# Kernel optimization log

Measured on AMD Instinct MI355X. Metric: run time of the kernel, lower is better.

## Reference

```python
import jax, jax.numpy as jnp
import numpy as np

B, N, R, DIM = 4, 1024, 5, 1024
H, DH = 16, 64
ALPHA = 128.0
# FLAGS.fix_attention=True, a_sim=False: q * (dim_head**-0.5 * alpha**-1) * mult**-0.5
SCALE = (DH ** -0.5) * (1.0 / ALPHA) * (R ** -0.5)
EPS = 1e-5


def layernorm(x, g):
    mean = jnp.mean(x, axis=-1, keepdims=True)
    var = jnp.mean((x - mean) ** 2, axis=-1, keepdims=True)  # unbiased=False
    return (x - mean) * jax.lax.rsqrt(var + EPS) * g


def setup_inputs() -> dict:
    key = jax.random.key(0)
    ks = jax.random.split(key, 8)
    x = jax.random.normal(ks[0], (B, N, R, DIM), dtype=jnp.float32)
    mask = jax.random.bernoulli(ks[1], 0.9, (B, N))
    g_in = jnp.ones((DIM,), dtype=jnp.float32)
    Wq = jax.random.normal(ks[2], (DIM, H * DH), dtype=jnp.float32) * 0.02
    Wkv = jax.random.normal(ks[3], (DIM, 2 * DH), dtype=jnp.float32) * 0.02
    null_kv = jax.random.normal(ks[4], (2, DH), dtype=jnp.float32)
    Wout = jax.random.normal(ks[5], (H * DH, DIM), dtype=jnp.float32) * 0.02
    g_out = jnp.ones((DIM,), dtype=jnp.float32)
    return {"x": x, "mask": mask, "g_in": g_in, "Wq": Wq, "Wkv": Wkv,
            "null_kv": null_kv, "Wout": Wout, "g_out": g_out}


def reference(x, mask, g_in, Wq, Wkv, null_kv, Wout, g_out):
    # context defaults to the UN-normalized x (set before norm in the original)
    context = x
    xn = layernorm(x, g_in)                               # [b,n,r,dim]
    q = jnp.einsum('bnrc,ce->bnre', xn, Wq)               # [b,n,r,h*d]
    q = q.reshape(B, N, R, H, DH).transpose(0, 3, 1, 2, 4)  # b h n r d
    q = q * SCALE
    kv = jnp.einsum('bnrc,ce->bnre', context, Wkv)        # [b,n,r,2d] (multi-query: 1 kv head)
    k, v = kv[..., :DH], kv[..., DH:]                     # [b,n,r,d]
    # null kv token prepended along the j (sequence) axis, repeated over r
    nk = jnp.broadcast_to(null_kv[0], (B, 1, R, DH))
    nv = jnp.broadcast_to(null_kv[1], (B, 1, R, DH))
    k = jnp.concatenate([nk, k], axis=1)                  # [b,n+1,r,d]
    v = jnp.concatenate([nv, v], axis=1)
    sim = jnp.einsum('bhird,bjrd->bhij', q, k)            # [b,h,n,n+1]
    big = jnp.finfo(sim.dtype).max
    maskp = jnp.pad(mask, ((0, 0), (1, 0)), constant_values=True)  # null token always visible
    sim = jnp.where(maskp[:, None, None, :], sim, -big)
    # pb-relax: subtract detached row max, rescale by alpha
    sim = sim - jax.lax.stop_gradient(jnp.max(sim, axis=-1, keepdims=True))
    attn = jax.nn.softmax(sim * ALPHA, axis=-1)
    out = jnp.einsum('bhij,bjrd->bhird', attn, v)         # b h n r d
    out = out.transpose(0, 2, 3, 1, 4).reshape(B, N, R, H * DH)
    out = jnp.einsum('bnre,eo->bnro', out, Wout)
    return layernorm(out, g_out)
```

## Files before the change

### kernel.cpp

```cpp
#include <hip/hip_runtime.h>

#define B_   4
#define N_   1024
#define R_   5
#define DIM_ 1024
#define H_   16
#define DH_  64
#define NJ   1056
#define CDIM 320
#define MROWS (B_*N_*R_)

typedef unsigned int u32;
typedef unsigned short u16;
typedef __attribute__((ext_vector_type(8))) short bf16x8;
typedef __attribute__((ext_vector_type(4))) float f32x4;
typedef __attribute__((ext_vector_type(16))) float f32x16;

constexpr float SCALEA_ = 0.05590169943749474f;

__device__ __forceinline__ u16 f2bf(float f) {
  u32 u = __builtin_bit_cast(u32, f);
  u32 r = (u + 0x7fffu + ((u >> 16) & 1u)) >> 16;
  return (u16)r;
}
__device__ __forceinline__ u32 pack2(float lo, float hi) {
  return (u32)f2bf(lo) | ((u32)f2bf(hi) << 16);
}
__device__ __forceinline__ void gld_lds16(void* lds, const void* g) {
  __builtin_amdgcn_global_load_lds((const __attribute__((address_space(1))) u32*)g,
                                   (__attribute__((address_space(3))) u32*)lds, 16, 0, 0);
}

__global__ void mask_detect(const u32* __restrict__ m, int* __restrict__ flag) {
  int t = threadIdx.x;
  int fl = 0;
  for (int i = t; i < 1024; i += 256) {
    u32 wv = m[i];
    if (wv == 0x3f800000u) fl |= 4;
    else if (wv > 1u) fl |= 2;
    if ((i & 1) && wv == 1u) fl |= 1;
  }
  if (fl) atomicOr(flag, fl);
}

__global__ void build_bias(const void* __restrict__ mask, const int* __restrict__ flag,
                           float* __restrict__ biasg) {
  int idx = blockIdx.x * 256 + threadIdx.x;
  if (idx >= B_ * NJ) return;
  int b = idx / NJ, j = idx % NJ;
  int mv;
  if (j == 0) mv = 1;
  else if (j > N_) mv = 0;
  else {
    int fb = flag[0];
    int mode = (fb & 4) ? 2 : ((fb & 2) ? 1 : ((fb & 1) ? 0 : 3));
    int mi = b * N_ + (j - 1);
    if (mode == 0)      mv = ((const int*)mask)[mi] != 0;
    else if (mode == 1) mv = ((const unsigned char*)mask)[mi] != 0;
    else if (mode == 2) mv = ((const float*)mask)[mi] != 0.0f;
    else                mv = ((const int*)mask)[mi * 2] != 0;
  }
  biasg[idx] = mv ? 0.0f : -__builtin_inff();
}

__global__ void kvfill(const float* __restrict__ nullkv, u16* __restrict__ kg, u16* __restrict__ vTg) {
  int idx = blockIdx.x * 256 + threadIdx.x;
  if (idx >= B_ * 32 * CDIM) return;
  int c  = idx % CDIM;
  int jj = (idx / CDIM) & 31;
  int b  = idx / (CDIM * 32);
  int j  = (jj == 0) ? 0 : (1024 + jj);
  u16 kvv, vvv;
  if (jj == 0) { kvv = f2bf(nullkv[c & 63]); vvv = f2bf(nullkv[64 + (c & 63)]); }
  else         { kvv = 0; vvv = 0; }
  kg [(size_t)(b * NJ + j) * CDIM + c] = kvv;
  vTg[(((size_t)b * 33 + (j >> 5)) * CDIM + c) * 32 + (j & 31)] = vvv;
}

__global__ __launch_bounds__(256) void transpose_cast(const float* __restrict__ W,
                                                      u16* __restrict__ WT, int K, int Nn) {
  __shared__ float tile[32][33];
  int tx = threadIdx.x & 31, ty = threadIdx.x >> 5;
  int n0 = blockIdx.x * 32, k0 = blockIdx.y * 32;
  #pragma unroll
  for (int e = 0; e < 4; ++e)
    tile[ty + e * 8][tx] = W[(size_t)(k0 + ty + e * 8) * Nn + n0 + tx];
  __syncthreads();
  #pragma unroll
  for (int e = 0; e < 4; ++e)
    WT[(size_t)(n0 + ty + e * 8) * K + k0 + tx] = f2bf(tile[tx][ty + e * 8]);
}

__global__ __launch_bounds__(256) void ln_in(const float* __restrict__ x, const float* __restrict__ gin,
                                             u16* __restrict__ xn, u16* __restrict__ xb) {
  const size_t row = blockIdx.x;
  const int t = threadIdx.x, w = t >> 6, lane = t & 63;
  const float* xr = x + row * 1024;
  f32x4 v = *(const f32x4*)(xr + t * 4);
  float s = v[0] + v[1] + v[2] + v[3];
  #pragma unroll
  for (int o = 1; o < 64; o <<= 1) s += __shfl_xor(s, o);
  __shared__ float red[8];
  if (lane == 0) red[w] = s;
  __syncthreads();
  float mean = (red[0] + red[1] + red[2] + red[3]) * (1.0f / 1024.0f);
  f32x4 d;
  float ss = 0.f;
  #pragma unroll
  for (int e = 0; e < 4; ++e) { d[e] = v[e] - mean; ss += d[e] * d[e]; }
  #pragma unroll
  for (int o = 1; o < 64; o <<= 1) ss += __shfl_xor(ss, o);
  if (lane == 0) red[4 + w] = ss;
  __syncthreads();
  float var = (red[4] + red[5] + red[6] + red[7]) * (1.0f / 1024.0f);
  float rs = rsqrtf(var + 1e-5f);
  f32x4 gv = *(const f32x4*)(gin + t * 4);
  uint2 o1, o2;
  o1.x = pack2(d[0] * rs * gv[0], d[1] * rs * gv[1]);
  o1.y = pack2(d[2] * rs * gv[2], d[3] * rs * gv[3]);
  o2.x = pack2(v[0], v[1]);
  o2.y = pack2(v[2], v[3]);
  *(uint2*)(xn + row * 1024 + t * 4) = o1;
  *(uint2*)(xb + row * 1024 + t * 4) = o2;
}

__global__ __launch_bounds__(256) void ln_out(float* __restrict__ y, const float* __restrict__ gout) {
  const size_t row = blockIdx.x;
  const int t = threadIdx.x, w = t >> 6, lane = t & 63;
  float* yr = y + row * 1024;
  f32x4 v = *(const f32x4*)(yr + t * 4);
  float s = v[0] + v[1] + v[2] + v[3];
  #pragma unroll
  for (int o = 1; o < 64; o <<= 1) s += __shfl_xor(s, o);
  __shared__ float red[8];
  if (lane == 0) red[w] = s;
  __syncthreads();
  float mean = (red[0] + red[1] + red[2] + red[3]) * (1.0f / 1024.0f);
  f32x4 d;
  float ss = 0.f;
  #pragma unroll
  for (int e = 0; e < 4; ++e) { d[e] = v[e] - mean; ss += d[e] * d[e]; }
  #pragma unroll
  for (int o = 1; o < 64; o <<= 1) ss += __shfl_xor(ss, o);
  if (lane == 0) red[4 + w] = ss;
  __syncthreads();
  float var = (red[4] + red[5] + red[6] + red[7]) * (1.0f / 1024.0f);
  float rs = rsqrtf(var + 1e-5f);
  f32x4 gv = *(const f32x4*)(gout + t * 4);
  f32x4 o;
  #pragma unroll
  for (int e = 0; e < 4; ++e) o[e] = d[e] * rs * gv[e];
  *(f32x4*)(yr + t * 4) = o;
}

template <int EPI>
__global__ __launch_bounds__(256) void gemm_bt(const u16* __restrict__ A, const u16* __restrict__ BT,
                                               void* __restrict__ C0, void* __restrict__ C1,
                                               const int K, const int Nn) {
  __shared__ __align__(16) u16 As[128 * 32];
  __shared__ __align__(16) u16 Bs[128 * 32];
  const int t = threadIdx.x, w = t >> 6, lane = t & 63;
  const int g = lane >> 4, i16 = lane & 15;
  const int wr = w >> 1, wc = w & 1;
  const size_t m0 = (size_t)blockIdx.y * 128;
  const size_t n0 = (size_t)blockIdx.x * 128;
  const u16* Ab = A + m0 * K;
  const u16* Bb = BT + n0 * K;
  f32x4 acc[4][4];
  #pragma unroll
  for (int mi = 0; mi < 4; ++mi)
    #pragma unroll
    for (int ni = 0; ni < 4; ++ni) acc[mi][ni] = (f32x4){0.f, 0.f, 0.f, 0.f};

  for (int k0 = 0; k0 < K; k0 += 32) {
    __syncthreads();
    #pragma unroll
    for (int s = 0; s < 2; ++s) {
      int c = s * 256 + t;
      gld_lds16(&As[(s * 256 + w * 64) * 8], Ab + (size_t)(c >> 2) * K + k0 + (c & 3) * 8);
      gld_lds16(&Bs[(s * 256 + w * 64) * 8], Bb + (size_t)(c >> 2) * K + k0 + (c & 3) * 8);
    }
    __syncthreads();
    bf16x8 af[4], bfr[4];
    #pragma unroll
    for (int mi = 0; mi < 4; ++mi) af[mi]  = *(const bf16x8*)&As[(wr * 64 + mi * 16 + i16) * 32 + g * 8];
    #pragma unroll
    for (int ni = 0; ni < 4; ++ni) bfr[ni] = *(const bf16x8*)&Bs[(wc * 64 + ni * 16 + i16) * 32 + g * 8];
    #pragma unroll
    for (int mi = 0; mi < 4; ++mi)
      #pragma unroll
      for (int ni = 0; ni < 4; ++ni)
        acc[mi][ni] = __builtin_amdgcn_mfma_f32_16x16x32_bf16(af[mi], bfr[ni], acc[mi][ni], 0, 0, 0);
  }

  #pragma unroll
  for (int mi = 0; mi < 4; ++mi)
    #pragma unroll
    for (int ni = 0; ni < 4; ++ni)
      #pragma unroll
      for (int reg = 0; reg < 4; ++reg) {
        size_t gr = m0 + wr * 64 + mi * 16 + g * 4 + reg;
        int gc = (int)n0 + wc * 64 + ni * 16 + i16;
        float v = acc[mi][ni][reg];
        if (EPI == 0) {
          ((u16*)C0)[gr * 1024 + gc] = f2bf(v * SCALEA_);
        } else if (EPI == 1) {
          int grr = (int)gr;
          int b = grr / (N_ * R_);
          int rem = grr - b * (N_ * R_);
          int n = rem / R_;
          int r = rem - n * R_;
          int j = n + 1;
          u16 val = f2bf(v);
          if (gc < DH_) ((u16*)C0)[(size_t)(b * NJ + j) * CDIM + r * 64 + gc] = val;
          else ((u16*)C1)[(((size_t)b * 33 + (j >> 5)) * CDIM + r * 64 + (gc - DH_)) * 32 + (j & 31)] = val;
        } else {
          ((float*)C0)[gr * 1024 + gc] = v;
        }
      }
}

__global__ __launch_bounds__(256) void attn_kernel(const u16* __restrict__ qb, const u16* __restrict__ kg,
                                                   const u16* __restrict__ vTg, const float* __restrict__ biasg,
                                                   u16* __restrict__ attout) {
  const int blk0 = blockIdx.x;
  const int blk = (blk0 & 7) * 64 + (blk0 >> 3);
  const int it = blk & 7;
  const int h  = (blk >> 3) & 15;
  const int b  = blk >> 7;
  const int t = threadIdx.x;
  const int w = t >> 6, lane = t & 63;
  const int l31 = lane & 31, lh = lane >> 5;
  const int i0 = it * 128 + w * 32;

  __shared__ __align__(16) char Kl[2][20480];
  __shared__ __align__(16) char Vl[2][20480];

  int ksrc[5], vsrc[5];
  #pragma unroll
  for (int s = 0; s < 5; ++s) {
    int d = w * 320 + s * 64 + lane;
    int j = d / 40, c16 = d - j * 40;
    ksrc[s] = j * 640 + ((c16 ^ (j & 7)) << 4);
    int vc = d >> 2;
    vsrc[s] = vc * 64 + (((d & 3) ^ (vc & 3)) << 4);
  }
  const char* ktile = (const char*)(kg + (size_t)b * NJ * CDIM);
  const char* vtile = (const char*)(vTg + (size_t)b * 33 * CDIM * 32);

  bf16x8 qf[20];
  {
    const u16* qrow = qb + ((size_t)(b * N_ + i0 + l31) * R_) * 1024 + h * 64 + lh * 8;
    #pragma unroll
    for (int kk = 0; kk < 20; ++kk) {
      int k16 = kk * 16;
      qf[kk] = *(const bf16x8*)(qrow + (k16 >> 6) * 1024 + (k16 & 63));
    }
  }

  const float* bptr = biasg + b * NJ + lh * 4;

  f32x16 O[10];
  #pragma unroll
  for (int cf = 0; cf < 10; ++cf)
    #pragma unroll
    for (int r = 0; r < 16; ++r) O[cf][r] = 0.f;
  float d_run = 0.f;

  #pragma unroll
  for (int s = 0; s < 5; ++s) {
    gld_lds16(&Kl[0][w * 5120 + s * 1024], ktile + ksrc[s]);
    gld_lds16(&Vl[0][w * 5120 + s * 1024], vtile + vsrc[s]);
  }

  const int swz  = (l31 & 7) << 4;
  const int swzv = (l31 & 3) << 4;

  for (int jt = 0; jt < 33; ++jt) {
    const int cur = jt & 1;
    __syncthreads();

    if (jt + 1 < 33) {
      const char* kt1 = ktile + (size_t)(jt + 1) * 20480;
      const char* vt1 = vtile + (size_t)(jt + 1) * 20480;
      char* kd = &Kl[cur ^ 1][w * 5120];
      char* vd = &Vl[cur ^ 1][w * 5120];
      #pragma unroll
      for (int s = 0; s < 5; ++s) {
        gld_lds16(kd + s * 1024, kt1 + ksrc[s]);
        gld_lds16(vd + s * 1024, vt1 + vsrc[s]);
      }
    }

    const char* Kb  = &Kl[cur][0] + l31 * 640;
    const char* kb0 = Kb + ((0x00 | (lh << 4)) ^ swz);
    const char* kb1 = Kb + ((0x20 | (lh << 4)) ^ swz);
    const char* kb2 = Kb + ((0x40 | (lh << 4)) ^ swz);
    const char* kb3 = Kb + ((0x60 | (lh << 4)) ^ swz);
    f32x16 S0, S1;
    #pragma unroll
    for (int r = 0; r < 16; ++r) { S0[r] = 0.f; S1[r] = 0.f; }
    __builtin_amdgcn_s_setprio(1);
    #pragma unroll
    for (int kk = 0; kk < 20; ++kk) {
      const char* kb = ((kk & 3) == 0) ? kb0 : ((kk & 3) == 1) ? kb1 : ((kk & 3) == 2) ? kb2 : kb3;
      bf16x8 kf = *(const bf16x8*)(kb + (kk >> 2) * 128);
      if (kk & 1) S1 = __builtin_amdgcn_mfma_f32_32x32x16_bf16(kf, qf[kk], S1, 0, 0, 0);
      else        S0 = __builtin_amdgcn_mfma_f32_32x32x16_bf16(kf, qf[kk], S0, 0, 0, 0);
    }
    __builtin_amdgcn_s_setprio(0);

    f32x4 bb0 = *(const f32x4*)(bptr + (size_t)jt * 32 + 0);
    f32x4 bb1 = *(const f32x4*)(bptr + (size_t)jt * 32 + 8);
    f32x4 bb2 = *(const f32x4*)(bptr + (size_t)jt * 32 + 16);
    f32x4 bb3 = *(const f32x4*)(bptr + (size_t)jt * 32 + 24);
    float p[16];
    float ts = 0.f;
    #pragma unroll
    for (int r = 0; r < 16; ++r) {
      float bv = (r < 4) ? bb0[r & 3] : (r < 8) ? bb1[r & 3] : (r < 12) ? bb2[r & 3] : bb3[r & 3];
      float L = fminf(S0[r] + S1[r] + bv, 60.0f);
      p[r] = __expf(L);
      ts += p[r];
    }
    d_run += ts;

    u32 pk0 = pack2(p[0], p[1]),   pk1 = pack2(p[2], p[3]);
    u32 pk2 = pack2(p[4], p[5]),   pk3 = pack2(p[6], p[7]);
    u32 pk4 = pack2(p[8], p[9]),   pk5 = pack2(p[10], p[11]);
    u32 pk6 = pack2(p[12], p[13]), pk7 = pack2(p[14], p[15]);
    asm volatile("v_permlane32_swap_b32 %0, %1" : "+v"(pk0), "+v"(pk2));
    asm volatile("v_permlane32_swap_b32 %0, %1" : "+v"(pk1), "+v"(pk3));
    asm volatile("v_permlane32_swap_b32 %0, %1" : "+v"(pk4), "+v"(pk6));
    asm volatile("v_permlane32_swap_b32 %0, %1" : "+v"(pk5), "+v"(pk7));
    union { u32 u[4]; bf16x8 v; } f1, f2;
    f1.u[0] = pk0; f1.u[1] = pk1; f1.u[2] = pk2; f1.u[3] = pk3;
    f2.u[0] = pk4; f2.u[1] = pk5; f2.u[2] = pk6; f2.u[3] = pk7;

    const char* Vb  = &Vl[cur][0] + l31 * 64;
    const char* vb1 = Vb + ((lh << 4) ^ swzv);
    const char* vb2 = Vb + ((((lh ^ 2) << 4)) ^ swzv);
    __builtin_amdgcn_s_setprio(1);
    #pragma unroll
    for (int cf = 0; cf < 10; ++cf) {
      bf16x8 v0 = *(const bf16x8*)(vb1 + cf * 2048);
      bf16x8 v1 = *(const bf16x8*)(vb2 + cf * 2048);
      O[cf] = __builtin_amdgcn_mfma_f32_32x32x16_bf16(f1.v, v0, O[cf], 0, 0, 0);
      O[cf] = __builtin_amdgcn_mfma_f32_32x32x16_bf16(f2.v, v1, O[cf], 0, 0, 0);
    }
    __builtin_amdgcn_s_setprio(0);
  }

  d_run += __shfl_xor(d_run, 32);
  float inv = 1.0f / d_run;
  float invr[16];
  #pragma unroll
  for (int r = 0; r < 16; ++r) invr[r] = __shfl(inv, (r & 3) + 8 * (r >> 2) + 4 * lh);

  #pragma unroll
  for (int r = 0; r < 16; ++r) {
    int gi = i0 + (r & 3) + 8 * (r >> 2) + 4 * lh;
    u16* orow = attout + ((size_t)(b * N_ + gi) * R_) * 1024 + h * 64;
    #pragma unroll
    for (int cf = 0; cf < 10; ++cf) {
      int c = cf * 32 + l31;
      orow[(c >> 6) * 1024 + (c & 63)] = f2bf(O[cf][r] * invr[r]);
    }
  }
}

extern "C" void kernel_launch(void* const* d_in, const int* in_sizes, int n_in,
                              void* d_out, int out_size, void* d_ws, size_t ws_size,
                              hipStream_t stream) {
  (void)in_sizes; (void)n_in; (void)out_size; (void)ws_size;
  const float* x      = (const float*)d_in[0];
  const void*  mask   = d_in[1];
  const float* g_in   = (const float*)d_in[2];
  const float* Wq     = (const float*)d_in[3];
  const float* Wkv    = (const float*)d_in[4];
  const float* nullkv = (const float*)d_in[5];
  const float* Wout   = (const float*)d_in[6];
  const float* g_out  = (const float*)d_in[7];
  float* out = (float*)d_out;

  char* base = (char*)d_ws;
  size_t off = 0;
  auto carve = [&](size_t bytes) { char* r = base + off; off += (bytes + 255) & ~(size_t)255; return r; };
  int*   flag  = (int*)carve(4);
  float* biasg = (float*)carve((size_t)B_ * NJ * 4);
  u16* WqT   = (u16*)carve((size_t)1024 * 1024 * 2);
  u16* WkvT  = (u16*)carve((size_t)128 * 1024 * 2);
  u16* WoutT = (u16*)carve((size_t)1024 * 1024 * 2);
  u16* xn    = (u16*)carve((size_t)MROWS * 1024 * 2);
  u16* xb    = (u16*)carve((size_t)MROWS * 1024 * 2);
  u16* qb    = (u16*)carve((size_t)MROWS * 1024 * 2);
  u16* kg    = (u16*)carve((size_t)B_ * NJ * CDIM * 2);
  u16* vTg   = (u16*)carve((size_t)B_ * 33 * CDIM * 32 * 2);
  u16* attout = xn;

  hipMemsetAsync(flag, 0, 4, stream);
  mask_detect<<<1, 256, 0, stream>>>((const u32*)mask, flag);
  build_bias<<<(B_ * NJ + 255) / 256, 256, 0, stream>>>(mask, flag, biasg);
  kvfill<<<(B_ * 32 * CDIM + 255) / 256, 256, 0, stream>>>(nullkv, kg, vTg);
  transpose_cast<<<dim3(32, 32), 256, 0, stream>>>(Wq, WqT, 1024, 1024);
  transpose_cast<<<dim3(4, 32), 256, 0, stream>>>(Wkv, WkvT, 1024, 128);
  transpose_cast<<<dim3(32, 32), 256, 0, stream>>>(Wout, WoutT, 1024, 1024);
  ln_in<<<MROWS, 256, 0, stream>>>(x, g_in, xn, xb);
  gemm_bt<0><<<dim3(8, 160), 256, 0, stream>>>(xn, WqT, qb, nullptr, 1024, 1024);
  gemm_bt<1><<<dim3(1, 160), 256, 0, stream>>>(xb, WkvT, kg, vTg, 1024, 128);
  attn_kernel<<<512, 256, 0, stream>>>(qb, kg, vTg, biasg, attout);
  gemm_bt<2><<<dim3(8, 160), 256, 0, stream>>>(attout, WoutT, out, nullptr, 1024, 1024);
  ln_out<<<MROWS, 256, 0, stream>>>(out, g_out);
}
```

Baseline: 454.4 us.

## Single-buffer V tile loaded per step and add XOR swizzle to reduce bank conflicts

V is now kept in a single LDS buffer instead of a double buffer, which cuts LDS use from 80KB to 60KB per block and may allow more blocks per CU. Each step issues the V load for the current tile together with the K prefetch for the next one, then waits with partial vmcnt counts and an extra barrier before the PV MFMAs, so the V load overlaps the QK and softmax work. The K and V LDS swizzles also get an extra XOR term on the higher row bits, meant to cut bank conflicts. In exchange there is a second barrier per step, and V latency is exposed whenever QK finishes before the load arrives.

New measurement: 452.2 us. No clear change (-0.5%).

```diff
diff --git a/kernel.cpp b/kernel.cpp
--- a/kernel.cpp
+++ b/kernel.cpp
@@ -234,16 +234,18 @@
   const int i0 = it * 128 + w * 32;
 
   __shared__ __align__(16) char Kl[2][20480];
-  __shared__ __align__(16) char Vl[2][20480];
+  __shared__ __align__(16) char Vl[20480];
 
   int ksrc[5], vsrc[5];
   #pragma unroll
   for (int s = 0; s < 5; ++s) {
     int d = w * 320 + s * 64 + lane;
     int j = d / 40, c16 = d - j * 40;
-    ksrc[s] = j * 640 + ((c16 ^ (j & 7)) << 4);
-    int vc = d >> 2;
-    vsrc[s] = vc * 64 + (((d & 3) ^ (vc & 3)) << 4);
+    int fj = (j & 7) ^ (j >> 3);
+    ksrc[s] = j * 640 + ((c16 ^ fj) << 4);
+    int vc = d >> 2, sl = d & 3;
+    int gv = (vc & 3) ^ ((vc >> 3) & 3);
+    vsrc[s] = vc * 64 + ((sl ^ gv) << 4);
   }
   const char* ktile = (const char*)(kg + (size_t)b * NJ * CDIM);
   const char* vtile = (const char*)(vTg + (size_t)b * 33 * CDIM * 32);
@@ -268,35 +270,37 @@
   float d_run = 0.f;
 
   #pragma unroll
-  for (int s = 0; s < 5; ++s) {
+  for (int s = 0; s < 5; ++s)
     gld_lds16(&Kl[0][w * 5120 + s * 1024], ktile + ksrc[s]);
-    gld_lds16(&Vl[0][w * 5120 + s * 1024], vtile + vsrc[s]);
-  }
-
-  const int swz  = (l31 & 7) << 4;
-  const int swzv = (l31 & 3) << 4;
+
+  const int swzK = ((l31 & 7) ^ (l31 >> 3)) << 4;
+  const int swzV = ((l31 & 3) ^ ((l31 >> 3) & 3)) << 4;
 
   for (int jt = 0; jt < 33; ++jt) {
     const int cur = jt & 1;
-    __syncthreads();
-
-    if (jt + 1 < 33) {
+
+    asm volatile("s_waitcnt vmcnt(0)" ::: "memory");
+    __builtin_amdgcn_s_barrier();
+    __builtin_amdgcn_sched_barrier(0);
+
+    {
+      const char* vt = vtile + (size_t)jt * 20480;
+      #pragma unroll
+      for (int s = 0; s < 5; ++s)
+        gld_lds16(&Vl[w * 5120 + s * 1024], vt + vsrc[s]);
+    }
+    if (jt < 32) {
       const char* kt1 = ktile + (size_t)(jt + 1) * 20480;
-      const char* vt1 = vtile + (size_t)(jt + 1) * 20480;
-      char* kd = &Kl[cur ^ 1][w * 5120];
-      char* vd = &Vl[cur ^ 1][w * 5120];
       #pragma unroll
-      for (int s = 0; s < 5; ++s) {
-        gld_lds16(kd + s * 1024, kt1 + ksrc[s]);
-        gld_lds16(vd + s * 1024, vt1 + vsrc[s]);
-      }
+      for (int s = 0; s < 5; ++s)
+        gld_lds16(&Kl[cur ^ 1][w * 5120 + s * 1024], kt1 + ksrc[s]);
     }
 
     const char* Kb  = &Kl[cur][0] + l31 * 640;
-    const char* kb0 = Kb + ((0x00 | (lh << 4)) ^ swz);
-    const char* kb1 = Kb + ((0x20 | (lh << 4)) ^ swz);
-    const char* kb2 = Kb + ((0x40 | (lh << 4)) ^ swz);
-    const char* kb3 = Kb + ((0x60 | (lh << 4)) ^ swz);
+    const char* kb0 = Kb + ((0x00 | (lh << 4)) ^ swzK);
+    const char* kb1 = Kb + ((0x20 | (lh << 4)) ^ swzK);
+    const char* kb2 = Kb + ((0x40 | (lh << 4)) ^ swzK);
+    const char* kb3 = Kb + ((0x60 | (lh << 4)) ^ swzK);
     f32x16 S0, S1;
     #pragma unroll
     for (int r = 0; r < 16; ++r) { S0[r] = 0.f; S1[r] = 0.f; }
@@ -337,9 +341,14 @@
     f1.u[0] = pk0; f1.u[1] = pk1; f1.u[2] = pk2; f1.u[3] = pk3;
     f2.u[0] = pk4; f2.u[1] = pk5; f2.u[2] = pk6; f2.u[3] = pk7;
 
-    const char* Vb  = &Vl[cur][0] + l31 * 64;
-    const char* vb1 = Vb + ((lh << 4) ^ swzv);
-    const char* vb2 = Vb + ((((lh ^ 2) << 4)) ^ swzv);
+    if (jt < 32) asm volatile("s_waitcnt vmcnt(5)" ::: "memory");
+    else         asm volatile("s_waitcnt vmcnt(0)" ::: "memory");
+    __builtin_amdgcn_s_barrier();
+    __builtin_amdgcn_sched_barrier(0);
+
+    const char* Vb  = &Vl[0] + l31 * 64;
+    const char* vb1 = Vb + ((lh << 4) ^ swzV);
+    const char* vb2 = Vb + (((lh ^ 2) << 4) ^ swzV);
     __builtin_amdgcn_s_setprio(1);
     #pragma unroll
     for (int cf = 0; cf < 10; ++cf) {
```
